# Optimization experiments

Hardware: AMD Instinct MI355X
Metric: run time of the kernel (lower is better)

The kernel has to match this reference:

```python
import jax, jax.numpy as jnp
import numpy as np

DIM = 384
K = 64               # num_classes
TEMP = 0.1
BASE_TEMP = 2.0
LAMB = 25.0
PIXEL_SIZE = 50      # pixel_update_freq * 5
K_BAN = 10
SINKHORN_ITERS = 3
BS, N = 16, 512


def _l2norm(x, eps=1e-12):
    return x / jnp.maximum(jnp.linalg.norm(x, axis=-1, keepdims=True), eps)


def _online_clustering(scores):
    # SwAV-style Sinkhorn in log space on lamb-scaled cosine logits, then argmax.
    logq = scores
    for _ in range(SINKHORN_ITERS):
        logq = logq - jax.scipy.special.logsumexp(logq, axis=1, keepdims=True)
        logq = logq - jax.scipy.special.logsumexp(logq, axis=0, keepdims=True)
    return jnp.argmax(logq, axis=1)


def _supcon(anchor, y_anchor, contrast, y_contrast, exclude_diag, require_pos):
    # mask[i,j] = 1 if same label
    mask = (y_anchor[:, None] == y_contrast[None, :]).astype(anchor.dtype)
    logits = (anchor @ contrast.T) / TEMP
    logits = logits - jax.lax.stop_gradient(jnp.max(logits, axis=1, keepdims=True))
    if exclude_diag:
        mask = mask * (1.0 - jnp.eye(anchor.shape[0], dtype=anchor.dtype))
    exp_logits = jnp.exp(logits)
    # note: neg_mask = 1 - mask, so for exclude_diag the self term counts as negative (faithful)
    neg = (exp_logits * (1.0 - mask)).sum(axis=1, keepdims=True)
    log_prob = logits - jnp.log(exp_logits + neg)
    pos_cnt = mask.sum(axis=1)
    num = (mask * log_prob).sum(axis=1)
    if require_pos:
        valid = (pos_cnt > 0).astype(anchor.dtype)
        mlpp = jnp.where(pos_cnt > 0, num / jnp.maximum(pos_cnt, 1.0), 0.0)
        return -(TEMP / BASE_TEMP) * jnp.sum(mlpp) / jnp.maximum(valid.sum(), 1.0)
    return jnp.mean(-(TEMP / BASE_TEMP) * num / pos_cnt)


def _forward(feats, off_feats, cluster_center, point_queue):
    bs, n, dim = off_feats.shape
    n_off = _l2norm(off_feats.reshape(-1, dim))
    cluster_feats = jnp.concatenate([n_off, point_queue.reshape(-1, dim)], axis=0)
    log_alpha = cluster_feats @ cluster_center.T              # (bs*n + K*PIXEL_SIZE, K)
    labels = _online_clustering(log_alpha * LAMB)[: bs * n]
    f = _l2norm(feats).reshape(-1, dim)
    # ppc2: anchors vs sampled queue entries (same random column indices for every class)
    k_samp = PIXEL_SIZE - K_BAN
    idx = jax.random.permutation(jax.random.key(1), PIXEL_SIZE)[:k_samp]
    x_c = point_queue[:, idx, :].reshape(-1, dim)             # (K*k_samp, dim)
    y_c = jnp.repeat(jnp.arange(K), k_samp)
    loss = _supcon(f, labels, x_c, y_c, exclude_diag=False, require_pos=False)
    # ppc: anchors vs anchors, diagonal removed from positives
    loss = loss + _supcon(f, labels, f, labels, exclude_diag=True, require_pos=True)
    return loss


def setup_inputs() -> dict:
    key = jax.random.key(0)
    k1, k2, k3, k4 = jax.random.split(key, 4)
    feats = jax.random.normal(k1, (BS, N, DIM), dtype=jnp.float32)
    off_feats = jax.random.normal(k2, (BS, N, DIM), dtype=jnp.float32)
    cluster_center = _l2norm(jax.random.normal(k3, (K, DIM), dtype=jnp.float32))
    point_queue = _l2norm(jax.random.normal(k4, (K, PIXEL_SIZE, DIM), dtype=jnp.float32))
    return {"feats": feats, "off_feats": off_feats,
            "cluster_center": cluster_center, "point_queue": point_queue}


def reference(feats, off_feats, cluster_center, point_queue):
    return _forward(feats, off_feats, cluster_center, point_queue)
```

## Files before the change

### kernel.cpp

```cpp
#include <hip/hip_runtime.h>
#include <stdint.h>
#include <algorithm>

#define DIM   384
#define KCLS  64
#define NPIX  50
#define KSAMP 40
#define NANCH 8192
#define NQ    3200
#define NTOT  11392
#define NXC   2560

typedef __attribute__((ext_vector_type(8)))  short s16x8;
typedef __attribute__((ext_vector_type(16))) float f32x16;

struct Idx40 { int v[KSAMP]; };

__device__ __forceinline__ float wave_sum64(float v){
  #pragma unroll
  for (int o = 32; o >= 1; o >>= 1) v += __shfl_xor(v, o);
  return v;
}

__device__ __forceinline__ unsigned short f2bf(float x){
  union { float f; uint32_t u; } c; c.f = x;
  uint32_t r = c.u + 0x7FFFu + ((c.u >> 16) & 1u);
  if ((c.u & 0x7F800000u) == 0x7F800000u) r = c.u;
  return (unsigned short)(r >> 16);
}

__device__ __forceinline__ float bf2f(unsigned short h){
  union { uint32_t u; float f; } c; c.u = ((uint32_t)h) << 16;
  return c.f;
}

__device__ __forceinline__ void split_hl(float x, unsigned short& hi, unsigned short& lo){
  hi = f2bf(x);
  lo = f2bf(x - bf2f(hi));
}

__device__ __forceinline__ void gload16(const unsigned short* g, unsigned short* l){
  __builtin_amdgcn_global_load_lds(
      (const __attribute__((address_space(1))) unsigned int*)g,
      (__attribute__((address_space(3))) unsigned int*)l, 16, 0, 0);
}

__global__ __launch_bounds__(256) void norm_copy_k(const float* __restrict__ feats,
    const float* __restrict__ off, const float* __restrict__ pq,
    const float* __restrict__ CC,
    unsigned short* __restrict__ fNh,
    unsigned short* __restrict__ CFhi, unsigned short* __restrict__ CFlo,
    unsigned short* __restrict__ cchi, unsigned short* __restrict__ cclo,
    unsigned short* __restrict__ xch, Idx40 idx){
  int row  = blockIdx.x * 4 + (threadIdx.x >> 6);
  int lane = threadIdx.x & 63;
  if (row < 2 * NANCH){
    const float* src = (row < NANCH) ? feats + (size_t)row * DIM
                                     : off + (size_t)(row - NANCH) * DIM;
    float v[6]; float ss = 0.f;
    #pragma unroll
    for (int e = 0; e < 6; e++){ v[e] = src[lane + 64 * e]; ss += v[e] * v[e]; }
    ss = wave_sum64(ss);
    float inv = 1.f / fmaxf(sqrtf(ss), 1e-12f);
    if (row < NANCH){
      unsigned short* dh = fNh + (size_t)row * DIM;
      #pragma unroll
      for (int e = 0; e < 6; e++) dh[lane + 64 * e] = f2bf(v[e] * inv);
    } else {
      size_t base = (size_t)(row - NANCH) * DIM;
      #pragma unroll
      for (int e = 0; e < 6; e++){
        unsigned short h, l;
        split_hl(v[e] * inv, h, l);
        CFhi[base + lane + 64 * e] = h;
        CFlo[base + lane + 64 * e] = l;
      }
    }
  } else if (row < 2 * NANCH + NQ){
    int q = row - 2 * NANCH;
    const float* src = pq + (size_t)q * DIM;
    size_t base = (size_t)(NANCH + q) * DIM;
    #pragma unroll
    for (int e = 0; e < 6; e++){
      unsigned short h, l;
      split_hl(src[lane + 64 * e], h, l);
      CFhi[base + lane + 64 * e] = h;
      CFlo[base + lane + 64 * e] = l;
    }
  } else if (row < 2 * NANCH + NQ + KCLS){
    int r = row - 2 * NANCH - NQ;
    size_t base = (size_t)r * DIM;
    #pragma unroll
    for (int e = 0; e < 6; e++){
      unsigned short h, l;
      split_hl(CC[base + lane + 64 * e], h, l);
      cchi[base + lane + 64 * e] = h;
      cclo[base + lane + 64 * e] = l;
    }
  } else {
    int q = row - 2 * NANCH - NQ - KCLS;
    int c = q / KSAMP, t = q - c * KSAMP;
    const float* src = pq + ((size_t)c * NPIX + idx.v[t]) * DIM;
    unsigned short* dst = xch + (size_t)q * DIM;
    #pragma unroll
    for (int e = 0; e < 6; e++) dst[lane + 64 * e] = f2bf(src[lane + 64 * e]);
  }
}

__global__ __launch_bounds__(256) void gemm_logq_mfma_k(
    const unsigned short* __restrict__ Ahi, const unsigned short* __restrict__ Alo,
    const unsigned short* __restrict__ Bhi, const unsigned short* __restrict__ Blo,
    float* __restrict__ logq){
  __shared__ unsigned short lAh[128 * 64], lAl[128 * 64];
  __shared__ unsigned short lBh[64 * 64],  lBl[64 * 64];
  int t = threadIdx.x;
  int lane = t & 63, w = t >> 6;
  int l31 = lane & 31, half = lane >> 5;
  int i0 = blockIdx.x * 128;

  int rA = w * 32 + l31;
  int swA = ((rA & 7) << 4);
  int rB0 = l31, rB1 = 32 + l31;
  int swB = ((l31 & 7) << 4);

  f32x16 acc0, acc1;
  #pragma unroll
  for (int r = 0; r < 16; r++){ acc0[r] = 0.f; acc1[r] = 0.f; }

  for (int kc = 0; kc < 6; kc++){
    __syncthreads();
    #pragma unroll
    for (int p = 0; p < 4; p++){
      int c = t + p * 256;
      int row = c >> 3, col = c & 7;
      int sw = ((col << 4) ^ ((row & 7) << 4));
      *(s16x8*)((char*)lAh + row * 128 + sw) =
          *(const s16x8*)(Ahi + (size_t)(i0 + row) * DIM + kc * 64 + col * 8);
      *(s16x8*)((char*)lAl + row * 128 + sw) =
          *(const s16x8*)(Alo + (size_t)(i0 + row) * DIM + kc * 64 + col * 8);
    }
    #pragma unroll
    for (int p = 0; p < 2; p++){
      int c = t + p * 256;
      int row = c >> 3, col = c & 7;
      int sw = ((col << 4) ^ ((row & 7) << 4));
      *(s16x8*)((char*)lBh + row * 128 + sw) =
          *(const s16x8*)(Bhi + (size_t)row * DIM + kc * 64 + col * 8);
      *(s16x8*)((char*)lBl + row * 128 + sw) =
          *(const s16x8*)(Blo + (size_t)row * DIM + kc * 64 + col * 8);
    }
    __syncthreads();
    #pragma unroll
    for (int kk = 0; kk < 4; kk++){
      int kb = kk * 32 + half * 16;
      s16x8 fah  = *(const s16x8*)((char*)lAh + rA * 128 + (kb ^ swA));
      s16x8 fal  = *(const s16x8*)((char*)lAl + rA * 128 + (kb ^ swA));
      s16x8 fb0h = *(const s16x8*)((char*)lBh + rB0 * 128 + (kb ^ swB));
      s16x8 fb0l = *(const s16x8*)((char*)lBl + rB0 * 128 + (kb ^ swB));
      s16x8 fb1h = *(const s16x8*)((char*)lBh + rB1 * 128 + (kb ^ swB));
      s16x8 fb1l = *(const s16x8*)((char*)lBl + rB1 * 128 + (kb ^ swB));
      acc0 = __builtin_amdgcn_mfma_f32_32x32x16_bf16(fah, fb0h, acc0, 0, 0, 0);
      acc0 = __builtin_amdgcn_mfma_f32_32x32x16_bf16(fah, fb0l, acc0, 0, 0, 0);
      acc0 = __builtin_amdgcn_mfma_f32_32x32x16_bf16(fal, fb0h, acc0, 0, 0, 0);
      acc1 = __builtin_amdgcn_mfma_f32_32x32x16_bf16(fah, fb1h, acc1, 0, 0, 0);
      acc1 = __builtin_amdgcn_mfma_f32_32x32x16_bf16(fah, fb1l, acc1, 0, 0, 0);
      acc1 = __builtin_amdgcn_mfma_f32_32x32x16_bf16(fal, fb1h, acc1, 0, 0, 0);
    }
  }
  #pragma unroll
  for (int r = 0; r < 16; r++){
    int rowp = (r & 3) + 8 * (r >> 2) + 4 * half;
    size_t row = (size_t)(i0 + w * 32 + rowp);
    logq[row * KCLS + l31]      = 25.f * acc0[r];
    logq[row * KCLS + 32 + l31] = 25.f * acc1[r];
  }
}

__global__ __launch_bounds__(256) void rowpass_k(float* __restrict__ logq,
    const float* __restrict__ colsum, int useCol){
  int row  = blockIdx.x * 4 + (threadIdx.x >> 6);
  int lane = threadIdx.x & 63;
  float v = logq[(size_t)row * KCLS + lane];
  if (useCol) v -= logf(colsum[lane]);
  float m = v;
  #pragma unroll
  for (int o = 32; o >= 1; o >>= 1) m = fmaxf(m, __shfl_xor(m, o));
  float s = expf(v - m);
  s = wave_sum64(s);
  logq[(size_t)row * KCLS + lane] = v - (m + logf(s));
}

__global__ __launch_bounds__(256) void colsum_k(const float* __restrict__ logq,
    float* __restrict__ cs){
  int r0 = blockIdx.x * 128;
  int t = threadIdx.x, lane = t & 63, grp = t >> 6;
  float acc = 0.f;
  for (int r = grp; r < 128; r += 4)
    acc += __expf(logq[(size_t)(r0 + r) * KCLS + lane]);
  __shared__ float red[4][64];
  red[grp][lane] = acc;
  __syncthreads();
  if (t < 64) atomicAdd(&cs[t], red[0][t] + red[1][t] + red[2][t] + red[3][t]);
}

__global__ __launch_bounds__(256) void argmax_k(const float* __restrict__ logq,
    const float* __restrict__ cs, int* __restrict__ labels, int* __restrict__ cnt){
  __shared__ float clog[KCLS];
  int t = threadIdx.x;
  if (t < KCLS) clog[t] = logf(cs[t]);
  __syncthreads();
  int i = blockIdx.x * 256 + t;
  if (i >= NANCH) return;
  float best = -INFINITY; int bj = 0;
  for (int j = 0; j < KCLS; j++){
    float v = logq[(size_t)i * KCLS + j] - clog[j];
    if (v > best){ best = v; bj = j; }
  }
  labels[i] = bj;
  atomicAdd(&cnt[bj], 1);
}

__global__ void scan_k(const int* cnt, int* offs, int* offw){
  if (threadIdx.x == 0){
    int acc = 0;
    for (int c = 0; c < KCLS; c++){ offs[c] = acc; offw[c] = acc; acc += cnt[c]; }
  }
}

__global__ __launch_bounds__(256) void scatter_k(const int* __restrict__ labels,
    int* offw, int* __restrict__ sorted, const float* __restrict__ S,
    const float* __restrict__ S2, float* __restrict__ Sp, float* __restrict__ S2p){
  int i = blockIdx.x * 256 + threadIdx.x;
  if (i >= NANCH) return;
  int p = atomicAdd(&offw[labels[i]], 1);
  sorted[p] = i;
  Sp[p]  = S[i];
  S2p[p] = S2[i];
}

__global__ __launch_bounds__(256) void sortrows_k(const unsigned short* __restrict__ fNh,
    const int* __restrict__ sorted, unsigned short* __restrict__ fNs){
  int p = blockIdx.x * 4 + (threadIdx.x >> 6);
  int lane = threadIdx.x & 63;
  int src = sorted[p];
  const uint32_t* s = (const uint32_t*)(fNh + (size_t)src * DIM);
  uint32_t* d = (uint32_t*)(fNs + (size_t)p * DIM);
  #pragma unroll
  for (int e = 0; e < 3; e++) d[lane + 64 * e] = s[lane + 64 * e];
}

__global__ __launch_bounds__(256) void rowsums2_k(
    const unsigned short* __restrict__ A, const unsigned short* __restrict__ Bself,
    const unsigned short* __restrict__ Bxc, float* __restrict__ S, float* __restrict__ S2){
  int bi = blockIdx.x;
  const unsigned short* Bp; float* dst;
  int bj0, njt; bool selfpart;
  if (blockIdx.y < 16){
    selfpart = true; Bp = Bself; dst = S;
    bj0 = bi + (int)blockIdx.y * 4;
    njt = 64 - bj0;
    if (njt <= 0) return;
    if (njt > 4) njt = 4;
  } else {
    selfpart = false; Bp = Bxc; dst = S2;
    bj0 = ((int)blockIdx.y - 16) * 4;
    njt = 4;
  }

  __shared__ unsigned short lds[2][2][128 * 64];
  int t = threadIdx.x, lane = t & 63, w = t >> 6;
  int wr = w >> 1, wc = w & 1;
  int l31 = lane & 31, half = lane >> 5;
  int i0 = bi * 128;
  int lrow = lane >> 3, srcslot = (lane & 7) ^ lrow;
  size_t loff = (size_t)lrow * DIM + srcslot * 8;

  int rA0 = wr * 64 + l31, rA1 = rA0 + 32;
  int rB0 = wc * 64 + l31, rB1 = rB0 + 32;
  int swA = ((rA0 & 7) << 4), swB = ((rB0 & 7) << 4);

  f32x16 s0, s1, a00, a01, a10, a11;
  #pragma unroll
  for (int r = 0; r < 16; r++){ s0[r] = 0.f; s1[r] = 0.f; }

  #pragma unroll
  for (int c = 0; c < 4; c++){
    int chunk = w * 4 + c;
    gload16(A  + (size_t)(i0         + chunk * 8) * DIM + loff, &lds[0][0][chunk * 512]);
    gload16(Bp + (size_t)(bj0 * 128  + chunk * 8) * DIM + loff, &lds[0][1][chunk * 512]);
  }
  __syncthreads();

  int total = njt * 6;
  int buf = 0;
  for (int s = 0; s < total; s++){
    int jt = s / 6, kc = s - jt * 6;
    if (s + 1 < total){
      int sn = s + 1;
      int jt1 = sn / 6, kc1 = sn - jt1 * 6;
      int j1 = (bj0 + jt1) * 128;
      int nb = buf ^ 1;
      #pragma unroll
      for (int c = 0; c < 4; c++){
        int chunk = w * 4 + c;
        gload16(A  + (size_t)(i0 + chunk * 8) * DIM + kc1 * 64 + loff, &lds[nb][0][chunk * 512]);
        gload16(Bp + (size_t)(j1 + chunk * 8) * DIM + kc1 * 64 + loff, &lds[nb][1][chunk * 512]);
      }
    }
    if (kc == 0){
      #pragma unroll
      for (int r = 0; r < 16; r++){ a00[r] = 0.f; a01[r] = 0.f; a10[r] = 0.f; a11[r] = 0.f; }
    }
    const char* bA = (const char*)&lds[buf][0][0];
    const char* bB = (const char*)&lds[buf][1][0];
    #pragma unroll
    for (int kk = 0; kk < 4; kk++){
      int kb = kk * 32 + half * 16;
      s16x8 fa0 = *(const s16x8*)(bA + rA0 * 128 + (kb ^ swA));
      s16x8 fa1 = *(const s16x8*)(bA + rA1 * 128 + (kb ^ swA));
      s16x8 fb0 = *(const s16x8*)(bB + rB0 * 128 + (kb ^ swB));
      s16x8 fb1 = *(const s16x8*)(bB + rB1 * 128 + (kb ^ swB));
      a00 = __builtin_amdgcn_mfma_f32_32x32x16_bf16(fa0, fb0, a00, 0, 0, 0);
      a01 = __builtin_amdgcn_mfma_f32_32x32x16_bf16(fa0, fb1, a01, 0, 0, 0);
      a10 = __builtin_amdgcn_mfma_f32_32x32x16_bf16(fa1, fb0, a10, 0, 0, 0);
      a11 = __builtin_amdgcn_mfma_f32_32x32x16_bf16(fa1, fb1, a11, 0, 0, 0);
    }
    if (kc == 5){
      int j0 = (bj0 + jt) * 128;
      bool docol = selfpart && (bj0 + jt != bi);
      float c0 = 0.f, c1 = 0.f;
      #pragma unroll
      for (int r = 0; r < 16; r++){
        float e00 = __expf(fmaf(a00[r], 10.f, -10.f));
        float e01 = __expf(fmaf(a01[r], 10.f, -10.f));
        float e10 = __expf(fmaf(a10[r], 10.f, -10.f));
        float e11 = __expf(fmaf(a11[r], 10.f, -10.f));
        s0[r] += e00 + e01;
        s1[r] += e10 + e11;
        c0 += e00 + e10;
        c1 += e01 + e11;
      }
      if (docol){
        c0 += __shfl_xor(c0, 32);
        c1 += __shfl_xor(c1, 32);
        if (half == 0){
          atomicAdd(&dst[j0 + wc * 64 + l31], c0);
          atomicAdd(&dst[j0 + wc * 64 + 32 + l31], c1);
        }
      }
    }
    __syncthreads();
    buf ^= 1;
  }

  #pragma unroll
  for (int o = 1; o < 32; o <<= 1){
    #pragma unroll
    for (int r = 0; r < 16; r++){
      s0[r] += __shfl_xor(s0[r], o);
      s1[r] += __shfl_xor(s1[r], o);
    }
  }
  if (l31 == 0){
    #pragma unroll
    for (int r = 0; r < 16; r++){
      int rowp = (r & 3) + 8 * (r >> 2) + 4 * half;
      atomicAdd(&dst[i0 + wr * 64 + rowp], s0[r]);
      atomicAdd(&dst[i0 + wr * 64 + 32 + rowp], s1[r]);
    }
  }
}

__device__ __forceinline__ void gram2(const s16x8* afr,
    const unsigned short* b0, const unsigned short* b1, f32x16& acc0, f32x16& acc1){
  #pragma unroll
  for (int ks = 0; ks < 24; ks++){
    s16x8 v0 = *(const s16x8*)(b0 + ks * 16);
    s16x8 v1 = *(const s16x8*)(b1 + ks * 16);
    acc0 = __builtin_amdgcn_mfma_f32_32x32x16_bf16(afr[ks], v0, acc0, 0, 0, 0);
    acc1 = __builtin_amdgcn_mfma_f32_32x32x16_bf16(afr[ks], v1, acc1, 0, 0, 0);
  }
}

__global__ __launch_bounds__(64) void classpair_k(
    const unsigned short* __restrict__ fNs, const unsigned short* __restrict__ xch,
    const int* __restrict__ offs, const int* __restrict__ cnt,
    const float* __restrict__ S, const float* __restrict__ S2,
    float* __restrict__ num2A, float* __restrict__ mlppA, float* __restrict__ validA){
  int c = blockIdx.x;
  int n = cnt[c], o0 = offs[c];
  if (n == 0) return;
  int lane = threadIdx.x;
  int l31 = lane & 31, half = lane >> 5;
  int ntiles = (n + 31) >> 5;

  for (int rt = blockIdx.y; rt < ntiles; rt += gridDim.y){
    int rpos = rt * 32 + l31;
    const unsigned short* arow = fNs + (size_t)(o0 + (rpos < n ? rpos : 0)) * DIM + half * 8;
    s16x8 afr[24];
    #pragma unroll
    for (int ks = 0; ks < 24; ks++) afr[ks] = *(const s16x8*)(arow + ks * 16);

    f32x16 p20, p21;
    #pragma unroll
    for (int r = 0; r < 16; r++){ p20[r] = 0.f; p21[r] = 0.f; }
    {
      int c1 = 32 + l31;
      const unsigned short* b0 = xch + ((size_t)c * KSAMP + l31) * DIM + half * 8;
      const unsigned short* b1 = xch + ((size_t)c * KSAMP + (c1 < KSAMP ? c1 : 0)) * DIM + half * 8;
      gram2(afr, b0, b1, p20, p21);
    }
    f32x16 red;
    #pragma unroll
    for (int r = 0; r < 16; r++){
      float v0 = expf(fmaf(p20[r], 10.f, -10.f));
      float v1 = (l31 < 8) ? expf(fmaf(p21[r], 10.f, -10.f)) : 0.f;
      red[r] = v0 + v1;
    }
    #pragma unroll
    for (int o = 1; o < 32; o <<= 1)
      #pragma unroll
      for (int r = 0; r < 16; r++) red[r] += __shfl_xor(red[r], o);
    float neg2[16];
    #pragma unroll
    for (int r = 0; r < 16; r++){
      int rowp = (r & 3) + 8 * (r >> 2) + 4 * half;
      int rp = rt * 32 + rowp;
      neg2[r] = (rp < n) ? S2[o0 + rp] - red[r] : 1.f;
    }
    #pragma unroll
    for (int r = 0; r < 16; r++){
      float l0 = fmaf(p20[r], 10.f, -10.f);
      float l1 = fmaf(p21[r], 10.f, -10.f);
      float a = l0 - logf(expf(l0) + neg2[r]);
      float b = (l31 < 8) ? l1 - logf(expf(l1) + neg2[r]) : 0.f;
      red[r] = a + b;
    }
    #pragma unroll
    for (int o = 1; o < 32; o <<= 1)
      #pragma unroll
      for (int r = 0; r < 16; r++) red[r] += __shfl_xor(red[r], o);
    if (l31 == 0){
      #pragma unroll
      for (int r = 0; r < 16; r++){
        int rowp = (r & 3) + 8 * (r >> 2) + 4 * half;
        int rp = rt * 32 + rowp;
        if (rp < n) num2A[o0 + rp] = red[r];
      }
    }

    f32x16 pe;
    #pragma unroll
    for (int r = 0; r < 16; r++) pe[r] = 0.f;
    for (int ct = 0; ct < ntiles; ct += 2){
      int cp0 = ct * 32 + l31;
      int cp1 = (ct + 1) * 32 + l31;
      bool has1 = (ct + 1) < ntiles;
      const unsigned short* b0 = fNs + (size_t)(o0 + (cp0 < n ? cp0 : 0)) * DIM + half * 8;
      const unsigned short* b1 = fNs + (size_t)(o0 + (has1 && cp1 < n ? cp1 : 0)) * DIM + half * 8;
      f32x16 a0, a1;
      #pragma unroll
      for (int r = 0; r < 16; r++){ a0[r] = 0.f; a1[r] = 0.f; }
      gram2(afr, b0, b1, a0, a1);
      #pragma unroll
      for (int r = 0; r < 16; r++){
        int rowp = (r & 3) + 8 * (r >> 2) + 4 * half;
        int rp = rt * 32 + rowp;
        if (cp0 < n && cp0 != rp) pe[r] += expf(fmaf(a0[r], 10.f, -10.f));
        if (has1 && cp1 < n && cp1 != rp) pe[r] += expf(fmaf(a1[r], 10.f, -10.f));
      }
    }
    #pragma unroll
    for (int o = 1; o < 32; o <<= 1)
      #pragma unroll
      for (int r = 0; r < 16; r++) pe[r] += __shfl_xor(pe[r], o);
    float neg[16];
    #pragma unroll
    for (int r = 0; r < 16; r++){
      int rowp = (r & 3) + 8 * (r >> 2) + 4 * half;
      int rp = rt * 32 + rowp;
      neg[r] = (rp < n) ? S[o0 + rp] - pe[r] : 1.f;
    }

    f32x16 nm;
    #pragma unroll
    for (int r = 0; r < 16; r++) nm[r] = 0.f;
    for (int ct = 0; ct < ntiles; ct += 2){
      int cp0 = ct * 32 + l31;
      int cp1 = (ct + 1) * 32 + l31;
      bool has1 = (ct + 1) < ntiles;
      const unsigned short* b0 = fNs + (size_t)(o0 + (cp0 < n ? cp0 : 0)) * DIM + half * 8;
      const unsigned short* b1 = fNs + (size_t)(o0 + (has1 && cp1 < n ? cp1 : 0)) * DIM + half * 8;
      f32x16 a0, a1;
      #pragma unroll
      for (int r = 0; r < 16; r++){ a0[r] = 0.f; a1[r] = 0.f; }
      gram2(afr, b0, b1, a0, a1);
      #pragma unroll
      for (int r = 0; r < 16; r++){
        int rowp = (r & 3) + 8 * (r >> 2) + 4 * half;
        int rp = rt * 32 + rowp;
        if (cp0 < n && cp0 != rp){
          float l = fmaf(a0[r], 10.f, -10.f);
          nm[r] += l - logf(expf(l) + neg[r]);
        }
        if (has1 && cp1 < n && cp1 != rp){
          float l = fmaf(a1[r], 10.f, -10.f);
          nm[r] += l - logf(expf(l) + neg[r]);
        }
      }
    }
    #pragma unroll
    for (int o = 1; o < 32; o <<= 1)
      #pragma unroll
      for (int r = 0; r < 16; r++) nm[r] += __shfl_xor(nm[r], o);
    if (l31 == 0){
      #pragma unroll
      for (int r = 0; r < 16; r++){
        int rowp = (r & 3) + 8 * (r >> 2) + 4 * half;
        int rp = rt * 32 + rowp;
        if (rp < n){
          if (n > 1){ mlppA[o0 + rp] = nm[r] / (float)(n - 1); validA[o0 + rp] = 1.f; }
          else      { mlppA[o0 + rp] = 0.f; validA[o0 + rp] = 0.f; }
        }
      }
    }
  }
}

__global__ __launch_bounds__(256) void finalize_k(const float* __restrict__ num2A,
    const float* __restrict__ mlppA, const float* __restrict__ validA,
    float* __restrict__ out){
  int t = threadIdx.x;
  float s2 = 0.f, sm = 0.f, sv = 0.f;
  for (int i = t; i < NANCH; i += 256){ s2 += num2A[i]; sm += mlppA[i]; sv += validA[i]; }
  __shared__ float a2[256], am[256], av[256];
  a2[t] = s2; am[t] = sm; av[t] = sv; __syncthreads();
  for (int o = 128; o >= 1; o >>= 1){
    if (t < o){ a2[t] += a2[t+o]; am[t] += am[t+o]; av[t] += av[t+o]; }
    __syncthreads();
  }
  if (t == 0){
    float loss1 = -0.05f * a2[0] / (40.f * (float)NANCH);
    float loss2 = -0.05f * am[0] / fmaxf(av[0], 1.f);
    out[0] = loss1 + loss2;
  }
}

static void tf2x32(uint32_t k0, uint32_t k1, uint32_t x0, uint32_t x1, uint32_t out[2]){
  uint32_t ks[3] = { k0, k1, k0 ^ k1 ^ 0x1BD11BDAu };
  static const int R[2][4] = { {13,15,26,6}, {17,29,16,24} };
  x0 += ks[0]; x1 += ks[1];
  for (int i = 0; i < 5; i++){
    for (int j = 0; j < 4; j++){
      x0 += x1;
      int r = R[i & 1][j];
      x1 = (x1 << r) | (x1 >> (32 - r));
      x1 ^= x0;
    }
    x0 += ks[(i + 1) % 3];
    x1 += ks[(i + 2) % 3] + (uint32_t)(i + 1);
  }
  out[0] = x0; out[1] = x1;
}

static void compute_idx(int idx_out[KSAMP]){
  uint32_t p0[2], p1[2];
  tf2x32(0u, 1u, 0u, 2u, p0);
  tf2x32(0u, 1u, 1u, 3u, p1);
  uint32_t sk0 = p0[1], sk1 = p1[1];
  uint32_t bits[NPIX];
  for (int i = 0; i < 25; i++){
    uint32_t o[2];
    tf2x32(sk0, sk1, (uint32_t)i, (uint32_t)(25 + i), o);
    bits[i] = o[0]; bits[25 + i] = o[1];
  }
  int perm[NPIX];
  for (int i = 0; i < NPIX; i++) perm[i] = i;
  std::stable_sort(perm, perm + NPIX, [&](int a, int b){ return bits[a] < bits[b]; });
  for (int i = 0; i < KSAMP; i++) idx_out[i] = perm[i];
}

extern "C" void kernel_launch(void* const* d_in, const int* in_sizes, int n_in,
                              void* d_out, int out_size, void* d_ws, size_t ws_size,
                              hipStream_t stream){
  const float* feats = (const float*)d_in[0];
  const float* off   = (const float*)d_in[1];
  const float* cc    = (const float*)d_in[2];
  const float* pq    = (const float*)d_in[3];
  float* out = (float*)d_out;

  char* ws = (char*)d_ws;
  size_t ofs = 0;
  auto alloc = [&](size_t bytes) -> void* {
    ofs = (ofs + 255) & ~(size_t)255;
    void* p = ws + ofs;
    ofs += bytes;
    return p;
  };
  float* logq   = (float*)alloc((size_t)NTOT * KCLS * 4);
  unsigned short* fNh  = (unsigned short*)alloc((size_t)NANCH * DIM * 2);
  unsigned short* fNs  = (unsigned short*)alloc((size_t)NANCH * DIM * 2);
  unsigned short* CFhi = (unsigned short*)alloc((size_t)NTOT * DIM * 2);
  unsigned short* CFlo = (unsigned short*)alloc((size_t)NTOT * DIM * 2);
  unsigned short* cchi = (unsigned short*)alloc((size_t)KCLS * DIM * 2);
  unsigned short* cclo = (unsigned short*)alloc((size_t)KCLS * DIM * 2);
  unsigned short* xch  = (unsigned short*)alloc((size_t)NXC * DIM * 2);
  float* S2     = (float*)alloc((2 * NANCH + KCLS + 3 * KCLS) * 4);
  float* S      = S2 + NANCH;
  int*   cnt    = (int*)(S2 + 2 * NANCH);
  float* cs0    = S2 + 2 * NANCH + KCLS;
  float* cs1    = cs0 + KCLS;
  float* cs2    = cs1 + KCLS;
  float* Sp     = (float*)alloc(NANCH * 4);
  float* S2p    = (float*)alloc(NANCH * 4);
  float* num2A  = (float*)alloc(NANCH * 4);
  float* mlppA  = (float*)alloc(NANCH * 4);
  float* validA = (float*)alloc(NANCH * 4);
  int* labels   = (int*)alloc(NANCH * 4);
  int* sorted   = (int*)alloc(NANCH * 4);
  int* offs     = (int*)alloc(KCLS * 4);
  int* offw     = (int*)alloc(KCLS * 4);

  Idx40 idx;
  compute_idx(idx.v);

  hipMemsetAsync(S2, 0, (2 * NANCH + 4 * KCLS) * 4, stream);
  norm_copy_k<<<(2 * NANCH + NQ + KCLS + NXC) / 4, 256, 0, stream>>>(
      feats, off, pq, cc, fNh, CFhi, CFlo, cchi, cclo, xch, idx);
  rowsums2_k<<<dim3(64, 21), 256, 0, stream>>>(fNh, fNh, xch, S, S2);
  gemm_logq_mfma_k<<<NTOT / 128, 256, 0, stream>>>(CFhi, CFlo, cchi, cclo, logq);
  rowpass_k<<<NTOT / 4, 256, 0, stream>>>(logq, cs0, 0);
  colsum_k<<<NTOT / 128, 256, 0, stream>>>(logq, cs0);
  rowpass_k<<<NTOT / 4, 256, 0, stream>>>(logq, cs0, 1);
  colsum_k<<<NTOT / 128, 256, 0, stream>>>(logq, cs1);
  rowpass_k<<<NTOT / 4, 256, 0, stream>>>(logq, cs1, 1);
  colsum_k<<<NTOT / 128, 256, 0, stream>>>(logq, cs2);
  argmax_k<<<NANCH / 256, 256, 0, stream>>>(logq, cs2, labels, cnt);
  scan_k<<<1, 64, 0, stream>>>(cnt, offs, offw);
  scatter_k<<<NANCH / 256, 256, 0, stream>>>(labels, offw, sorted, S, S2, Sp, S2p);
  sortrows_k<<<NANCH / 4, 256, 0, stream>>>(fNh, sorted, fNs);
  classpair_k<<<dim3(KCLS, 8), 64, 0, stream>>>(fNs, xch, offs, cnt, Sp, S2p,
                                                num2A, mlppA, validA);
  finalize_k<<<1, 256, 0, stream>>>(num2A, mlppA, validA, out);
}
```

Baseline: 252.6 us.

## Fuse Sinkhorn row pass with column sum and drop rowsums double buffering

New measurement: 297.7 us. +17.9%, slower.

```diff
diff --git a/kernel.cpp b/kernel.cpp
--- a/kernel.cpp
+++ b/kernel.cpp
@@ -176,31 +176,28 @@
   }
 }
 
-__global__ __launch_bounds__(256) void rowpass_k(float* __restrict__ logq,
-    const float* __restrict__ colsum, int useCol){
-  int row  = blockIdx.x * 4 + (threadIdx.x >> 6);
-  int lane = threadIdx.x & 63;
-  float v = logq[(size_t)row * KCLS + lane];
-  if (useCol) v -= logf(colsum[lane]);
-  float m = v;
-  #pragma unroll
-  for (int o = 32; o >= 1; o >>= 1) m = fmaxf(m, __shfl_xor(m, o));
-  float s = expf(v - m);
-  s = wave_sum64(s);
-  logq[(size_t)row * KCLS + lane] = v - (m + logf(s));
-}
-
-__global__ __launch_bounds__(256) void colsum_k(const float* __restrict__ logq,
-    float* __restrict__ cs){
+__global__ __launch_bounds__(256) void rowcol_k(float* __restrict__ logq,
+    const float* __restrict__ csPrev, float* __restrict__ csNext, int useCol){
   int r0 = blockIdx.x * 128;
   int t = threadIdx.x, lane = t & 63, grp = t >> 6;
-  float acc = 0.f;
-  for (int r = grp; r < 128; r += 4)
-    acc += __expf(logq[(size_t)(r0 + r) * KCLS + lane]);
+  float cl = useCol ? logf(csPrev[lane]) : 0.f;
+  float colacc = 0.f;
+  for (int r = grp; r < 128; r += 4){
+    size_t off = (size_t)(r0 + r) * KCLS + lane;
+    float v = logq[off] - cl;
+    float m = v;
+    #pragma unroll
+    for (int o = 32; o >= 1; o >>= 1) m = fmaxf(m, __shfl_xor(m, o));
+    float e = expf(v - m);
+    float s = wave_sum64(e);
+    float nv = v - (m + logf(s));
+    logq[off] = nv;
+    colacc += expf(nv);
+  }
   __shared__ float red[4][64];
-  red[grp][lane] = acc;
+  red[grp][lane] = colacc;
   __syncthreads();
-  if (t < 64) atomicAdd(&cs[t], red[0][t] + red[1][t] + red[2][t] + red[3][t]);
+  if (t < 64) atomicAdd(&csNext[t], red[0][t] + red[1][t] + red[2][t] + red[3][t]);
 }
 
 __global__ __launch_bounds__(256) void argmax_k(const float* __restrict__ logq,
@@ -267,7 +264,8 @@
     njt = 4;
   }
 
-  __shared__ unsigned short lds[2][2][128 * 64];
+  __shared__ unsigned short lA[128 * 64];
+  __shared__ unsigned short lB[128 * 64];
   int t = threadIdx.x, lane = t & 63, w = t >> 6;
   int wr = w >> 1, wc = w & 1;
   int l31 = lane & 31, half = lane >> 5;
@@ -283,36 +281,24 @@
   #pragma unroll
   for (int r = 0; r < 16; r++){ s0[r] = 0.f; s1[r] = 0.f; }
 
-  #pragma unroll
-  for (int c = 0; c < 4; c++){
-    int chunk = w * 4 + c;
-    gload16(A  + (size_t)(i0         + chunk * 8) * DIM + loff, &lds[0][0][chunk * 512]);
-    gload16(Bp + (size_t)(bj0 * 128  + chunk * 8) * DIM + loff, &lds[0][1][chunk * 512]);
-  }
-  __syncthreads();
-
   int total = njt * 6;
-  int buf = 0;
   for (int s = 0; s < total; s++){
     int jt = s / 6, kc = s - jt * 6;
-    if (s + 1 < total){
-      int sn = s + 1;
-      int jt1 = sn / 6, kc1 = sn - jt1 * 6;
-      int j1 = (bj0 + jt1) * 128;
-      int nb = buf ^ 1;
-      #pragma unroll
-      for (int c = 0; c < 4; c++){
-        int chunk = w * 4 + c;
-        gload16(A  + (size_t)(i0 + chunk * 8) * DIM + kc1 * 64 + loff, &lds[nb][0][chunk * 512]);
-        gload16(Bp + (size_t)(j1 + chunk * 8) * DIM + kc1 * 64 + loff, &lds[nb][1][chunk * 512]);
-      }
-    }
+    int j0 = (bj0 + jt) * 128;
+    __syncthreads();
+    #pragma unroll
+    for (int c = 0; c < 4; c++){
+      int chunk = w * 4 + c;
+      gload16(A  + (size_t)(i0 + chunk * 8) * DIM + kc * 64 + loff, &lA[chunk * 512]);
+      gload16(Bp + (size_t)(j0 + chunk * 8) * DIM + kc * 64 + loff, &lB[chunk * 512]);
+    }
+    __syncthreads();
     if (kc == 0){
       #pragma unroll
       for (int r = 0; r < 16; r++){ a00[r] = 0.f; a01[r] = 0.f; a10[r] = 0.f; a11[r] = 0.f; }
     }
-    const char* bA = (const char*)&lds[buf][0][0];
-    const char* bB = (const char*)&lds[buf][1][0];
+    const char* bA = (const char*)lA;
+    const char* bB = (const char*)lB;
     #pragma unroll
     for (int kk = 0; kk < 4; kk++){
       int kb = kk * 32 + half * 16;
@@ -326,7 +312,6 @@
       a11 = __builtin_amdgcn_mfma_f32_32x32x16_bf16(fa1, fb1, a11, 0, 0, 0);
     }
     if (kc == 5){
-      int j0 = (bj0 + jt) * 128;
       bool docol = selfpart && (bj0 + jt != bi);
       float c0 = 0.f, c1 = 0.f;
       #pragma unroll
@@ -349,8 +334,6 @@
         }
       }
     }
-    __syncthreads();
-    buf ^= 1;
   }
 
   #pragma unroll
@@ -629,12 +612,9 @@
       feats, off, pq, cc, fNh, CFhi, CFlo, cchi, cclo, xch, idx);
   rowsums2_k<<<dim3(64, 21), 256, 0, stream>>>(fNh, fNh, xch, S, S2);
   gemm_logq_mfma_k<<<NTOT / 128, 256, 0, stream>>>(CFhi, CFlo, cchi, cclo, logq);
-  rowpass_k<<<NTOT / 4, 256, 0, stream>>>(logq, cs0, 0);
-  colsum_k<<<NTOT / 128, 256, 0, stream>>>(logq, cs0);
-  rowpass_k<<<NTOT / 4, 256, 0, stream>>>(logq, cs0, 1);
-  colsum_k<<<NTOT / 128, 256, 0, stream>>>(logq, cs1);
-  rowpass_k<<<NTOT / 4, 256, 0, stream>>>(logq, cs1, 1);
-  colsum_k<<<NTOT / 128, 256, 0, stream>>>(logq, cs2);
+  rowcol_k<<<NTOT / 128, 256, 0, stream>>>(logq, cs0, cs0, 0);
+  rowcol_k<<<NTOT / 128, 256, 0, stream>>>(logq, cs0, cs1, 1);
+  rowcol_k<<<NTOT / 128, 256, 0, stream>>>(logq, cs1, cs2, 1);
   argmax_k<<<NANCH / 256, 256, 0, stream>>>(logq, cs2, labels, cnt);
   scan_k<<<1, 64, 0, stream>>>(cnt, offs, offw);
   scatter_k<<<NANCH / 256, 256, 0, stream>>>(labels, offw, sorted, S, S2, Sp, S2p);
```

## Balance symmetric self-similarity tiles with cyclic diagonal assignment in rowsums

Applied to the files above, without the earlier changes.

Result: faster. 239.0 us (median of 3 runs) (-5.4%).

```diff
diff --git a/kernel.cpp b/kernel.cpp
--- a/kernel.cpp
+++ b/kernel.cpp
@@ -250,21 +250,18 @@
 }
 
 __global__ __launch_bounds__(256) void rowsums2_k(
-    const unsigned short* __restrict__ A, const unsigned short* __restrict__ Bself,
-    const unsigned short* __restrict__ Bxc, float* __restrict__ S, float* __restrict__ S2){
-  int bi = blockIdx.x;
+    const unsigned short* __restrict__ A, const unsigned short* __restrict__ Bxc,
+    float* __restrict__ S, float* __restrict__ S2){
+  int bi = blockIdx.x, y = blockIdx.y;
   const unsigned short* Bp; float* dst;
-  int bj0, njt; bool selfpart;
-  if (blockIdx.y < 16){
-    selfpart = true; Bp = Bself; dst = S;
-    bj0 = bi + (int)blockIdx.y * 4;
-    njt = 64 - bj0;
-    if (njt <= 0) return;
-    if (njt > 4) njt = 4;
+  int d0 = 0, bjx0 = 0, njt; bool selfpart;
+  if (y < 8){
+    selfpart = true; Bp = A; dst = S; d0 = y * 4; njt = 4;
+  } else if (y == 8){
+    if (bi >= 32) return;
+    selfpart = true; Bp = A; dst = S; d0 = 32; njt = 1;
   } else {
-    selfpart = false; Bp = Bxc; dst = S2;
-    bj0 = ((int)blockIdx.y - 16) * 4;
-    njt = 4;
+    selfpart = false; Bp = Bxc; dst = S2; bjx0 = (y - 9) * 4; njt = 4;
   }
 
   __shared__ unsigned short lds[2][2][128 * 64];
@@ -279,15 +276,23 @@
   int rB0 = wc * 64 + l31, rB1 = rB0 + 32;
   int swA = ((rA0 & 7) << 4), swB = ((rB0 & 7) << 4);
 
+  auto jcol = [&](int jt) -> int {
+    if (selfpart){ int js = bi + d0 + jt; return (js & 63) * 128; }
+    return (bjx0 + jt) * 128;
+  };
+
   f32x16 s0, s1, a00, a01, a10, a11;
   #pragma unroll
   for (int r = 0; r < 16; r++){ s0[r] = 0.f; s1[r] = 0.f; }
 
-  #pragma unroll
-  for (int c = 0; c < 4; c++){
-    int chunk = w * 4 + c;
-    gload16(A  + (size_t)(i0         + chunk * 8) * DIM + loff, &lds[0][0][chunk * 512]);
-    gload16(Bp + (size_t)(bj0 * 128  + chunk * 8) * DIM + loff, &lds[0][1][chunk * 512]);
+  {
+    int j0 = jcol(0);
+    #pragma unroll
+    for (int c = 0; c < 4; c++){
+      int chunk = w * 4 + c;
+      gload16(A  + (size_t)(i0 + chunk * 8) * DIM + loff, &lds[0][0][chunk * 512]);
+      gload16(Bp + (size_t)(j0 + chunk * 8) * DIM + loff, &lds[0][1][chunk * 512]);
+    }
   }
   __syncthreads();
 
@@ -298,7 +303,7 @@
     if (s + 1 < total){
       int sn = s + 1;
       int jt1 = sn / 6, kc1 = sn - jt1 * 6;
-      int j1 = (bj0 + jt1) * 128;
+      int j1 = jcol(jt1);
       int nb = buf ^ 1;
       #pragma unroll
       for (int c = 0; c < 4; c++){
@@ -326,8 +331,8 @@
       a11 = __builtin_amdgcn_mfma_f32_32x32x16_bf16(fa1, fb1, a11, 0, 0, 0);
     }
     if (kc == 5){
-      int j0 = (bj0 + jt) * 128;
-      bool docol = selfpart && (bj0 + jt != bi);
+      int j0 = jcol(jt);
+      bool docol = selfpart && (d0 + jt != 0);
       float c0 = 0.f, c1 = 0.f;
       #pragma unroll
       for (int r = 0; r < 16; r++){
@@ -627,7 +632,7 @@
   hipMemsetAsync(S2, 0, (2 * NANCH + 4 * KCLS) * 4, stream);
   norm_copy_k<<<(2 * NANCH + NQ + KCLS + NXC) / 4, 256, 0, stream>>>(
       feats, off, pq, cc, fNh, CFhi, CFlo, cchi, cclo, xch, idx);
-  rowsums2_k<<<dim3(64, 21), 256, 0, stream>>>(fNh, fNh, xch, S, S2);
+  rowsums2_k<<<dim3(64, 14), 256, 0, stream>>>(fNh, xch, S, S2);
   gemm_logq_mfma_k<<<NTOT / 128, 256, 0, stream>>>(CFhi, CFlo, cchi, cclo, logq);
   rowpass_k<<<NTOT / 4, 256, 0, stream>>>(logq, cs0, 0);
   colsum_k<<<NTOT / 128, 256, 0, stream>>>(logq, cs0);
```
